# Kernel optimization log

Measured on AMD Instinct MI355X. Metric: run time of the kernel, lower is better.

The kernel has to match this reference:

```python
import jax, jax.numpy as jnp
import numpy as np

OUTDIM, INPUTDIM, DEGREE = 64, 512, 8


def setup_inputs() -> dict:
    key = jax.random.key(0)
    k1, k2 = jax.random.split(key)
    x = jax.random.normal(k1, (16, 4096, INPUTDIM), dtype=jnp.float32)
    # torch.randn(outdim, inputdim, degree) / (sqrt(inputdim)*sqrt(degree))
    coeffs = jax.random.normal(k2, (OUTDIM, INPUTDIM, DEGREE), dtype=jnp.float32)
    coeffs = coeffs / (np.sqrt(INPUTDIM) * np.sqrt(DEGREE))
    bias = jnp.zeros((1, OUTDIM), dtype=jnp.float32)
    return {"x": x, "coeffs": coeffs, "bias": bias}


def _legendre_basis(xn, degree):
    # Iterative (memoized) Legendre recurrence; xn in [-1, 1], shape [N, I].
    Ps = [jnp.ones_like(xn)]
    if degree > 1:
        Ps.append(xn)
    for n in range(2, degree):
        Ps.append(((2.0 * n - 1.0) * xn * Ps[-1] - (n - 1.0) * Ps[-2]) / n)
    return jnp.stack(Ps, axis=-1)  # [N, I, D]


def reference(x, coeffs, bias):
    outdim, inputdim, degree = coeffs.shape
    outshape = x.shape[:-1] + (outdim,)
    x2 = x.reshape(-1, inputdim)                      # [N, I]
    xmin, xmax = x2.min(), x2.max()                   # global min-max normalize
    xn = 2.0 * (x2 - xmin) / (xmax - xmin) - 1.0
    P = _legendre_basis(xn, degree)                   # [N, I, D]
    y = jnp.einsum("nid,oid->no", P, coeffs)          # contract input & degree
    y = y + bias                                      # [N, O]
    return y.reshape(outshape)
```

## Files before the change

kernel.cpp:

```cpp
#include <hip/hip_runtime.h>
#include <math.h>


typedef __bf16 bf16x8 __attribute__((ext_vector_type(8)));
typedef float f32x4 __attribute__((ext_vector_type(4)));

__global__ __launch_bounds__(256) void k_minmax_partial(
    const float4* __restrict__ x4, int n4, float* __restrict__ pmn, float* __restrict__ pmx)
{
  float mn = 3.4e38f, mx = -3.4e38f;
  int stride = gridDim.x * 256;
  for (int i = blockIdx.x * 256 + threadIdx.x; i < n4; i += stride) {
    float4 v = x4[i];
    mn = fminf(mn, fminf(fminf(v.x, v.y), fminf(v.z, v.w)));
    mx = fmaxf(mx, fmaxf(fmaxf(v.x, v.y), fmaxf(v.z, v.w)));
  }
  #pragma unroll
  for (int off = 32; off > 0; off >>= 1) {
    mn = fminf(mn, __shfl_down(mn, off));
    mx = fmaxf(mx, __shfl_down(mx, off));
  }
  __shared__ float smn[4], smx[4];
  int w = threadIdx.x >> 6;
  if ((threadIdx.x & 63) == 0) { smn[w] = mn; smx[w] = mx; }
  __syncthreads();
  if (threadIdx.x == 0) {
    pmn[blockIdx.x] = fminf(fminf(smn[0], smn[1]), fminf(smn[2], smn[3]));
    pmx[blockIdx.x] = fmaxf(fmaxf(smx[0], smx[1]), fmaxf(smx[2], smx[3]));
  }
}

__global__ __launch_bounds__(256) void k_minmax_final(
    const float* __restrict__ pmn, const float* __restrict__ pmx, int nb, float* __restrict__ so)
{
  float mn = 3.4e38f, mx = -3.4e38f;
  for (int i = threadIdx.x; i < nb; i += 256) {
    mn = fminf(mn, pmn[i]);
    mx = fmaxf(mx, pmx[i]);
  }
  #pragma unroll
  for (int off = 32; off > 0; off >>= 1) {
    mn = fminf(mn, __shfl_down(mn, off));
    mx = fmaxf(mx, __shfl_down(mx, off));
  }
  __shared__ float smn[4], smx[4];
  int w = threadIdx.x >> 6;
  if ((threadIdx.x & 63) == 0) { smn[w] = mn; smx[w] = mx; }
  __syncthreads();
  if (threadIdx.x == 0) {
    mn = fminf(fminf(smn[0], smn[1]), fminf(smn[2], smn[3]));
    mx = fmaxf(fmaxf(smx[0], smx[1]), fmaxf(smx[2], smx[3]));
    float r = mx - mn;
    so[0] = 2.0f / r;
    so[1] = -2.0f * mn / r - 1.0f;
  }
}

__global__ __launch_bounds__(256) void k_prepB(const float* __restrict__ coeffs,
                                               bf16x8* __restrict__ Bws)
{
  int t = blockIdx.x * 256 + threadIdx.x;
  int lane = t & 63;
  int tile = t >> 6;
  int ct = tile & 3;
  int kt = tile >> 2;
  int i = kt * 4 + (lane >> 4);
  int o = ct * 16 + (lane & 15);
  const float4* cp = (const float4*)(coeffs + ((size_t)o * 512 + i) * 8);
  float4 c0 = cp[0], c1 = cp[1];
  bf16x8 v;
  v[0] = (__bf16)c0.x; v[1] = (__bf16)c0.y; v[2] = (__bf16)c0.z; v[3] = (__bf16)c0.w;
  v[4] = (__bf16)c1.x; v[5] = (__bf16)c1.y; v[6] = (__bf16)c1.z; v[7] = (__bf16)c1.w;
  Bws[t] = v;
}

#define LSTRIDE 36
__global__ __launch_bounds__(128, 1) void k_main(
    const float* __restrict__ x, const bf16x8* __restrict__ Bws,
    const float* __restrict__ bias, const float* __restrict__ so,
    float* __restrict__ y)
{
  __shared__ float xs[2][128 * LSTRIDE];

  const float s = so[0], off = so[1];
  const int t    = threadIdx.x;
  const int lane = t & 63;
  const int w    = t >> 6;
  const int m    = lane & 15;
  const int quad = lane >> 4;
  const size_t blockRow = (size_t)blockIdx.x * 128;

  const int srow = t >> 3;
  const int scol = (t & 7) * 4;
  const float* xg = x + blockRow * 512;

  int rbase[4];
  #pragma unroll
  for (int f = 0; f < 4; ++f) rbase[f] = (w * 64 + f * 16 + m) * LSTRIDE + quad;

  const bf16x8* Bp = Bws + lane;

  f32x4 acc[4][4];
  #pragma unroll
  for (int f = 0; f < 4; ++f)
    #pragma unroll
    for (int ct = 0; ct < 4; ++ct) acc[f][ct] = (f32x4){0.f, 0.f, 0.f, 0.f};

  const float c3a = 5.f / 3.f,  c3b = 2.f / 3.f;
  const float c6a = 11.f / 6.f, c6b = 5.f / 6.f;
  const float c7a = 13.f / 7.f, c7b = 6.f / 7.f;

  {
    #pragma unroll
    for (int p = 0; p < 8; ++p) {
      float4 v = *(const float4*)(xg + (size_t)(srow + 16 * p) * 512 + scol);
      *(float4*)&xs[0][(srow + 16 * p) * LSTRIDE + scol] = v;
    }
  }
  __syncthreads();

  bf16x8 Bq[4][4];
  #pragma unroll
  for (int ct = 0; ct < 4; ++ct) {
    Bq[0][ct] = Bp[(size_t)(0 * 4 + ct) * 64];
    Bq[1][ct] = Bp[(size_t)(1 * 4 + ct) * 64];
  }

  for (int c = 0; c < 16; ++c) {
    const float* xr = xs[c & 1];
    float*       xw = xs[(c & 1) ^ 1];

    float4 st[8];
    if (c < 15) {
      const float* gp = xg + (c + 1) * 32;
      #pragma unroll
      for (int p = 0; p < 8; ++p)
        st[p] = *(const float4*)(gp + (size_t)(srow + 16 * p) * 512 + scol);
    }

    float xv[2][4];
    #pragma unroll
    for (int f = 0; f < 4; ++f) xv[0][f] = xr[rbase[f]];

    #pragma unroll
    for (int ktl = 0; ktl < 8; ++ktl) {
      const int kt = c * 8 + ktl;

      {
        const int kp = (kt + 2) & 127;
        const bf16x8* bpk = Bp + (size_t)kp * 256;
        #pragma unroll
        for (int ct = 0; ct < 4; ++ct) Bq[(ktl + 2) & 3][ct] = bpk[ct * 64];
      }
      if (ktl < 7) {
        #pragma unroll
        for (int f = 0; f < 4; ++f)
          xv[(ktl + 1) & 1][f] = xr[rbase[f] + (ktl + 1) * 4];
      }

      bf16x8 a[4];
      #pragma unroll
      for (int f = 0; f < 4; ++f) {
        float xn = fmaf(xv[ktl & 1][f], s, off);
        float p2 = fmaf(1.5f * xn, xn, -0.5f);
        float p3 = fmaf(c3a * xn, p2, -(c3b * xn));
        float p4 = fmaf(1.75f * xn, p3, -(0.75f * p2));
        float p5 = fmaf(1.8f * xn, p4, -(0.8f * p3));
        float p6 = fmaf(c6a * xn, p5, -(c6b * p4));
        float p7 = fmaf(c7a * xn, p6, -(c7b * p5));
        bf16x8 av;
        av[0] = (__bf16)1.0f; av[1] = (__bf16)xn; av[2] = (__bf16)p2; av[3] = (__bf16)p3;
        av[4] = (__bf16)p4;   av[5] = (__bf16)p5; av[6] = (__bf16)p6; av[7] = (__bf16)p7;
        a[f] = av;
      }

      #pragma unroll
      for (int f = 0; f < 4; ++f)
        #pragma unroll
        for (int ct = 0; ct < 4; ++ct)
          acc[f][ct] = __builtin_amdgcn_mfma_f32_16x16x32_bf16(a[f], Bq[ktl & 3][ct], acc[f][ct], 0, 0, 0);
    }

    if (c < 15) {
      #pragma unroll
      for (int p = 0; p < 8; ++p)
        *(float4*)&xw[(srow + 16 * p) * LSTRIDE + scol] = st[p];
    }
    __syncthreads();
  }

  float bv0 = bias[m], bv1 = bias[16 + m], bv2 = bias[32 + m], bv3 = bias[48 + m];
  #pragma unroll
  for (int f = 0; f < 4; ++f) {
    float* yp = y + (blockRow + w * 64 + f * 16 + quad * 4) * 64 + m;
    #pragma unroll
    for (int r = 0; r < 4; ++r) {
      float* ypr = yp + r * 64;
      ypr[0]  = acc[f][0][r] + bv0;
      ypr[16] = acc[f][1][r] + bv1;
      ypr[32] = acc[f][2][r] + bv2;
      ypr[48] = acc[f][3][r] + bv3;
    }
  }
}

__global__ __launch_bounds__(256) void k_main_simple(
    const float* __restrict__ x, const float* __restrict__ coeffs,
    const float* __restrict__ bias, const float* __restrict__ so, float* __restrict__ y)
{
  const float s = so[0], off = so[1];
  const int lane = threadIdx.x & 63;
  const int w    = threadIdx.x >> 6;
  const int m    = lane & 15;
  const int quad = lane >> 4;
  const int rowA = blockIdx.x * 64 + w * 16 + m;
  const float* xp = x + (size_t)rowA * 512 + quad;

  f32x4 acc0 = {0.f,0.f,0.f,0.f}, acc1 = acc0, acc2 = acc0, acc3 = acc0;
  const float c3a = 5.f/3.f, c3b = 2.f/3.f, c6a = 11.f/6.f, c6b = 5.f/6.f, c7a = 13.f/7.f, c7b = 6.f/7.f;

  for (int kt = 0; kt < 128; ++kt) {
    float xv = xp[kt * 4];
    int i = kt * 4 + quad;
    bf16x8 b[4];
    #pragma unroll
    for (int ct = 0; ct < 4; ++ct) {
      const float* cp = coeffs + ((size_t)(ct * 16 + m) * 512 + i) * 8;
      #pragma unroll
      for (int j = 0; j < 8; ++j) b[ct][j] = (__bf16)cp[j];
    }
    float xn = fmaf(xv, s, off);
    float p2 = fmaf(1.5f * xn, xn, -0.5f);
    float p3 = fmaf(c3a * xn, p2, -(c3b * xn));
    float p4 = fmaf(1.75f * xn, p3, -(0.75f * p2));
    float p5 = fmaf(1.8f * xn, p4, -(0.8f * p3));
    float p6 = fmaf(c6a * xn, p5, -(c6b * p4));
    float p7 = fmaf(c7a * xn, p6, -(c7b * p5));
    bf16x8 a;
    a[0] = (__bf16)1.0f; a[1] = (__bf16)xn; a[2] = (__bf16)p2; a[3] = (__bf16)p3;
    a[4] = (__bf16)p4;   a[5] = (__bf16)p5; a[6] = (__bf16)p6; a[7] = (__bf16)p7;
    acc0 = __builtin_amdgcn_mfma_f32_16x16x32_bf16(a, b[0], acc0, 0, 0, 0);
    acc1 = __builtin_amdgcn_mfma_f32_16x16x32_bf16(a, b[1], acc1, 0, 0, 0);
    acc2 = __builtin_amdgcn_mfma_f32_16x16x32_bf16(a, b[2], acc2, 0, 0, 0);
    acc3 = __builtin_amdgcn_mfma_f32_16x16x32_bf16(a, b[3], acc3, 0, 0, 0);
  }
  float b0v = bias[m], b1v = bias[16+m], b2v = bias[32+m], b3v = bias[48+m];
  float* yp = y + ((size_t)(blockIdx.x * 64 + w * 16 + quad * 4)) * 64 + m;
  #pragma unroll
  for (int r = 0; r < 4; ++r) {
    yp[r*64+ 0] = acc0[r] + b0v;
    yp[r*64+16] = acc1[r] + b1v;
    yp[r*64+32] = acc2[r] + b2v;
    yp[r*64+48] = acc3[r] + b3v;
  }
}

extern "C" void kernel_launch(void* const* d_in, const int* in_sizes, int n_in,
                              void* d_out, int out_size, void* d_ws, size_t ws_size,
                              hipStream_t stream)
{
  const float* x      = (const float*)d_in[0];
  const float* coeffs = (const float*)d_in[1];
  const float* bias   = (const float*)d_in[2];
  float* y = (float*)d_out;

  long nx = (long)in_sizes[0];
  int  N  = (int)(nx / 512);
  int  n4 = (int)(nx / 4);

  float*  so  = (float*)d_ws;
  float*  pmn = (float*)d_ws + 16;
  float*  pmx = pmn + 4096;
  bf16x8* Bws = (bf16x8*)((char*)d_ws + 65536);

  const int MMB = 2048;
  k_minmax_partial<<<MMB, 256, 0, stream>>>((const float4*)x, n4, pmn, pmx);
  k_minmax_final<<<1, 256, 0, stream>>>(pmn, pmx, MMB, so);

  bool pre = ws_size >= (size_t)(65536 + 4096 * 64 * 2 + 4096);
  if (pre) {
    k_prepB<<<128, 256, 0, stream>>>(coeffs, Bws);
    k_main<<<N / 128, 128, 0, stream>>>(x, Bws, bias, so, y);
  } else {
    k_main_simple<<<N / 64, 256, 0, stream>>>(x, coeffs, bias, so, y);
  }
}
```

Before: 287.5 us.

## Split K across waves with LDS reduction, merge prep kernels, rescale Legendre recurrence

The main kernel now uses 64-row blocks of 4 waves. Each wave handles a quarter of the input dimension over the same rows, stages its x slice in a private LDS buffer with no per-chunk barriers, and the partial accumulators are summed through shared memory at the end. The min-max finalize and coefficient conversion are merged into one launch. The Legendre recurrence is rewritten in monic (scaled) form, with the scale factors folded into the bf16 coefficients, which cuts the FLOPs per element. This aims to raise occupancy and parallelism, remove block-wide syncs and one launch, at the cost of an LDS reduction and a different bf16 rounding profile. The simple fallback path now reads unconverted coeffs while the prep kernel runs unconditionally, so the fallback still works.

```diff
diff --git a/kernel.cpp b/kernel.cpp
--- a/kernel.cpp
+++ b/kernel.cpp
@@ -30,57 +30,63 @@
   }
 }
 
-__global__ __launch_bounds__(256) void k_minmax_final(
-    const float* __restrict__ pmn, const float* __restrict__ pmx, int nb, float* __restrict__ so)
-{
-  float mn = 3.4e38f, mx = -3.4e38f;
-  for (int i = threadIdx.x; i < nb; i += 256) {
-    mn = fminf(mn, pmn[i]);
-    mx = fmaxf(mx, pmx[i]);
-  }
-  #pragma unroll
-  for (int off = 32; off > 0; off >>= 1) {
-    mn = fminf(mn, __shfl_down(mn, off));
-    mx = fmaxf(mx, __shfl_down(mx, off));
-  }
-  __shared__ float smn[4], smx[4];
-  int w = threadIdx.x >> 6;
-  if ((threadIdx.x & 63) == 0) { smn[w] = mn; smx[w] = mx; }
-  __syncthreads();
-  if (threadIdx.x == 0) {
-    mn = fminf(fminf(smn[0], smn[1]), fminf(smn[2], smn[3]));
-    mx = fmaxf(fmaxf(smx[0], smx[1]), fmaxf(smx[2], smx[3]));
-    float r = mx - mn;
-    so[0] = 2.0f / r;
-    so[1] = -2.0f * mn / r - 1.0f;
-  }
-}
-
-__global__ __launch_bounds__(256) void k_prepB(const float* __restrict__ coeffs,
-                                               bf16x8* __restrict__ Bws)
-{
-  int t = blockIdx.x * 256 + threadIdx.x;
-  int lane = t & 63;
-  int tile = t >> 6;
-  int ct = tile & 3;
-  int kt = tile >> 2;
-  int i = kt * 4 + (lane >> 4);
-  int o = ct * 16 + (lane & 15);
-  const float4* cp = (const float4*)(coeffs + ((size_t)o * 512 + i) * 8);
-  float4 c0 = cp[0], c1 = cp[1];
-  bf16x8 v;
-  v[0] = (__bf16)c0.x; v[1] = (__bf16)c0.y; v[2] = (__bf16)c0.z; v[3] = (__bf16)c0.w;
-  v[4] = (__bf16)c1.x; v[5] = (__bf16)c1.y; v[6] = (__bf16)c1.z; v[7] = (__bf16)c1.w;
-  Bws[t] = v;
-}
-
-#define LSTRIDE 36
-__global__ __launch_bounds__(128, 1) void k_main(
+__global__ __launch_bounds__(256) void k_prep_final(
+    const float* __restrict__ coeffs, bf16x8* __restrict__ Bws,
+    const float* __restrict__ pmn, const float* __restrict__ pmx, int nb,
+    float* __restrict__ so)
+{
+  if (blockIdx.x < 128) {
+    int t = blockIdx.x * 256 + threadIdx.x;
+    int lane = t & 63;
+    int tile = t >> 6;
+    int ct = tile & 3;
+    int kt = tile >> 2;
+    int i = kt * 4 + (lane >> 4);
+    int o = ct * 16 + (lane & 15);
+    const float4* cp = (const float4*)(coeffs + ((size_t)o * 512 + i) * 8);
+    float4 c0 = cp[0], c1 = cp[1];
+    bf16x8 v;
+    v[0] = (__bf16)(c0.x);
+    v[1] = (__bf16)(c0.y);
+    v[2] = (__bf16)(c0.z * 1.5f);
+    v[3] = (__bf16)(c0.w * 2.5f);
+    v[4] = (__bf16)(c1.x * 4.375f);
+    v[5] = (__bf16)(c1.y * 7.875f);
+    v[6] = (__bf16)(c1.z * 14.4375f);
+    v[7] = (__bf16)(c1.w * 26.8125f);
+    Bws[(size_t)(kt * 4 + ct) * 64 + lane] = v;
+  } else {
+    float mn = 3.4e38f, mx = -3.4e38f;
+    for (int i = threadIdx.x; i < nb; i += 256) {
+      mn = fminf(mn, pmn[i]);
+      mx = fmaxf(mx, pmx[i]);
+    }
+    #pragma unroll
+    for (int off = 32; off > 0; off >>= 1) {
+      mn = fminf(mn, __shfl_down(mn, off));
+      mx = fmaxf(mx, __shfl_down(mx, off));
+    }
+    __shared__ float smn[4], smx[4];
+    int w = threadIdx.x >> 6;
+    if ((threadIdx.x & 63) == 0) { smn[w] = mn; smx[w] = mx; }
+    __syncthreads();
+    if (threadIdx.x == 0) {
+      mn = fminf(fminf(smn[0], smn[1]), fminf(smn[2], smn[3]));
+      mx = fmaxf(fmaxf(smx[0], smx[1]), fmaxf(smx[2], smx[3]));
+      float r = mx - mn;
+      so[0] = 2.0f / r;
+      so[1] = -2.0f * mn / r - 1.0f;
+    }
+  }
+}
+
+#define LSTW 20
+__global__ __launch_bounds__(256, 3) void k_main(
     const float* __restrict__ x, const bf16x8* __restrict__ Bws,
     const float* __restrict__ bias, const float* __restrict__ so,
     float* __restrict__ y)
 {
-  __shared__ float xs[2][128 * LSTRIDE];
+  __shared__ char smem[49152];
 
   const float s = so[0], off = so[1];
   const int t    = threadIdx.x;
@@ -88,17 +94,16 @@
   const int w    = t >> 6;
   const int m    = lane & 15;
   const int quad = lane >> 4;
-  const size_t blockRow = (size_t)blockIdx.x * 128;
-
-  const int srow = t >> 3;
-  const int scol = (t & 7) * 4;
-  const float* xg = x + blockRow * 512;
-
-  int rbase[4];
-  #pragma unroll
-  for (int f = 0; f < 4; ++f) rbase[f] = (w * 64 + f * 16 + m) * LSTRIDE + quad;
-
-  const bf16x8* Bp = Bws + lane;
+  const size_t blockRow = (size_t)blockIdx.x * 64;
+
+  float* xsw = (float*)(smem + w * (2 * 64 * LSTW * 4));
+  const float* xg = x + (blockRow + lane) * 512 + w * 128;
+
+  int rb[4];
+  #pragma unroll
+  for (int f = 0; f < 4; ++f) rb[f] = (f * 16 + m) * LSTW + quad;
+
+  const bf16x8* Bp = Bws + (size_t)w * 32 * 256 + lane;
 
   f32x4 acc[4][4];
   #pragma unroll
@@ -106,71 +111,64 @@
     #pragma unroll
     for (int ct = 0; ct < 4; ++ct) acc[f][ct] = (f32x4){0.f, 0.f, 0.f, 0.f};
 
-  const float c3a = 5.f / 3.f,  c3b = 2.f / 3.f;
-  const float c6a = 11.f / 6.f, c6b = 5.f / 6.f;
-  const float c7a = 13.f / 7.f, c7b = 6.f / 7.f;
-
-  {
-    #pragma unroll
-    for (int p = 0; p < 8; ++p) {
-      float4 v = *(const float4*)(xg + (size_t)(srow + 16 * p) * 512 + scol);
-      *(float4*)&xs[0][(srow + 16 * p) * LSTRIDE + scol] = v;
-    }
-  }
-  __syncthreads();
+  const float C2 = 0.33333334f, C3 = 0.26666668f, C4 = 0.25714287f;
+  const float C5 = 0.25396827f, C6 = 0.25252524f, C7 = 0.25174826f;
+
+  float4 st[4];
+  #pragma unroll
+  for (int p = 0; p < 4; ++p) st[p] = *(const float4*)(xg + p * 4);
+  #pragma unroll
+  for (int p = 0; p < 4; ++p) *(float4*)&xsw[lane * LSTW + p * 4] = st[p];
 
   bf16x8 Bq[4][4];
   #pragma unroll
   for (int ct = 0; ct < 4; ++ct) {
-    Bq[0][ct] = Bp[(size_t)(0 * 4 + ct) * 64];
-    Bq[1][ct] = Bp[(size_t)(1 * 4 + ct) * 64];
-  }
-
-  for (int c = 0; c < 16; ++c) {
-    const float* xr = xs[c & 1];
-    float*       xw = xs[(c & 1) ^ 1];
-
-    float4 st[8];
-    if (c < 15) {
-      const float* gp = xg + (c + 1) * 32;
-      #pragma unroll
-      for (int p = 0; p < 8; ++p)
-        st[p] = *(const float4*)(gp + (size_t)(srow + 16 * p) * 512 + scol);
+    Bq[0][ct] = Bp[ct * 64];
+    Bq[1][ct] = Bp[256 + ct * 64];
+  }
+
+  for (int c = 0; c < 8; ++c) {
+    float* xr = xsw + (c & 1) * (64 * LSTW);
+
+    if (c < 7) {
+      const float* gp = xg + (c + 1) * 16;
+      #pragma unroll
+      for (int p = 0; p < 4; ++p) st[p] = *(const float4*)(gp + p * 4);
     }
 
     float xv[2][4];
     #pragma unroll
-    for (int f = 0; f < 4; ++f) xv[0][f] = xr[rbase[f]];
-
-    #pragma unroll
-    for (int ktl = 0; ktl < 8; ++ktl) {
-      const int kt = c * 8 + ktl;
+    for (int f = 0; f < 4; ++f) xv[0][f] = xr[rb[f]];
+
+    #pragma unroll
+    for (int ktl = 0; ktl < 4; ++ktl) {
+      const int l = c * 4 + ktl;
 
       {
-        const int kp = (kt + 2) & 127;
+        const int kp = (l + 2) & 31;
         const bf16x8* bpk = Bp + (size_t)kp * 256;
         #pragma unroll
         for (int ct = 0; ct < 4; ++ct) Bq[(ktl + 2) & 3][ct] = bpk[ct * 64];
       }
-      if (ktl < 7) {
+      if (ktl < 3) {
         #pragma unroll
         for (int f = 0; f < 4; ++f)
-          xv[(ktl + 1) & 1][f] = xr[rbase[f] + (ktl + 1) * 4];
+          xv[(ktl + 1) & 1][f] = xr[rb[f] + (ktl + 1) * 4];
       }
 
       bf16x8 a[4];
       #pragma unroll
       for (int f = 0; f < 4; ++f) {
         float xn = fmaf(xv[ktl & 1][f], s, off);
-        float p2 = fmaf(1.5f * xn, xn, -0.5f);
-        float p3 = fmaf(c3a * xn, p2, -(c3b * xn));
-        float p4 = fmaf(1.75f * xn, p3, -(0.75f * p2));
-        float p5 = fmaf(1.8f * xn, p4, -(0.8f * p3));
-        float p6 = fmaf(c6a * xn, p5, -(c6b * p4));
-        float p7 = fmaf(c7a * xn, p6, -(c7b * p5));
+        float s2 = fmaf(xn, xn, -C2);
+        float s3 = (s2 - C3) * xn;
+        float s4 = fmaf(xn, s3, -(C4 * s2));
+        float s5 = fmaf(xn, s4, -(C5 * s3));
+        float s6 = fmaf(xn, s5, -(C6 * s4));
+        float s7 = fmaf(xn, s6, -(C7 * s5));
         bf16x8 av;
-        av[0] = (__bf16)1.0f; av[1] = (__bf16)xn; av[2] = (__bf16)p2; av[3] = (__bf16)p3;
-        av[4] = (__bf16)p4;   av[5] = (__bf16)p5; av[6] = (__bf16)p6; av[7] = (__bf16)p7;
+        av[0] = (__bf16)1.0f; av[1] = (__bf16)xn; av[2] = (__bf16)s2; av[3] = (__bf16)s3;
+        av[4] = (__bf16)s4;   av[5] = (__bf16)s5; av[6] = (__bf16)s6; av[7] = (__bf16)s7;
         a[f] = av;
       }
 
@@ -181,25 +179,46 @@
           acc[f][ct] = __builtin_amdgcn_mfma_f32_16x16x32_bf16(a[f], Bq[ktl & 3][ct], acc[f][ct], 0, 0, 0);
     }
 
-    if (c < 15) {
-      #pragma unroll
-      for (int p = 0; p < 8; ++p)
-        *(float4*)&xw[(srow + 16 * p) * LSTRIDE + scol] = st[p];
-    }
-    __syncthreads();
-  }
-
-  float bv0 = bias[m], bv1 = bias[16 + m], bv2 = bias[32 + m], bv3 = bias[48 + m];
-  #pragma unroll
-  for (int f = 0; f < 4; ++f) {
-    float* yp = y + (blockRow + w * 64 + f * 16 + quad * 4) * 64 + m;
-    #pragma unroll
-    for (int r = 0; r < 4; ++r) {
-      float* ypr = yp + r * 64;
-      ypr[0]  = acc[f][0][r] + bv0;
-      ypr[16] = acc[f][1][r] + bv1;
-      ypr[32] = acc[f][2][r] + bv2;
-      ypr[48] = acc[f][3][r] + bv3;
+    if (c < 7) {
+      float* xw = xsw + ((c + 1) & 1) * (64 * LSTW);
+      #pragma unroll
+      for (int p = 0; p < 4; ++p) *(float4*)&xw[lane * LSTW + p * 4] = st[p];
+    }
+  }
+
+  __syncthreads();
+  f32x4* red = (f32x4*)smem;
+  if (w > 0) {
+    #pragma unroll
+    for (int f = 0; f < 4; ++f)
+      #pragma unroll
+      for (int ct = 0; ct < 4; ++ct)
+        red[(size_t)(w - 1) * 1024 + (f * 4 + ct) * 64 + lane] = acc[f][ct];
+  }
+  __syncthreads();
+  if (w == 0) {
+    #pragma unroll
+    for (int f = 0; f < 4; ++f)
+      #pragma unroll
+      for (int ct = 0; ct < 4; ++ct) {
+        f32x4 v = acc[f][ct];
+        v += red[(f * 4 + ct) * 64 + lane];
+        v += red[1024 + (f * 4 + ct) * 64 + lane];
+        v += red[2048 + (f * 4 + ct) * 64 + lane];
+        acc[f][ct] = v;
+      }
+    float bv0 = bias[m], bv1 = bias[16 + m], bv2 = bias[32 + m], bv3 = bias[48 + m];
+    #pragma unroll
+    for (int f = 0; f < 4; ++f) {
+      float* yp = y + (blockRow + f * 16 + quad * 4) * 64 + m;
+      #pragma unroll
+      for (int r = 0; r < 4; ++r) {
+        float* ypr = yp + r * 64;
+        ypr[0]  = acc[f][0][r] + bv0;
+        ypr[16] = acc[f][1][r] + bv1;
+        ypr[32] = acc[f][2][r] + bv2;
+        ypr[48] = acc[f][3][r] + bv3;
+      }
     }
   }
 }
@@ -275,12 +294,11 @@
 
   const int MMB = 2048;
   k_minmax_partial<<<MMB, 256, 0, stream>>>((const float4*)x, n4, pmn, pmx);
-  k_minmax_final<<<1, 256, 0, stream>>>(pmn, pmx, MMB, so);
 
   bool pre = ws_size >= (size_t)(65536 + 4096 * 64 * 2 + 4096);
+  k_prep_final<<<129, 256, 0, stream>>>(coeffs, Bws, pmn, pmx, MMB, so);
   if (pre) {
-    k_prepB<<<128, 256, 0, stream>>>(coeffs, Bws);
-    k_main<<<N / 128, 128, 0, stream>>>(x, Bws, bias, so, y);
+    k_main<<<N / 64, 256, 0, stream>>>(x, Bws, bias, so, y);
   } else {
     k_main_simple<<<N / 64, 256, 0, stream>>>(x, coeffs, bias, so, y);
   }
```

Measured after the change: 252.3 us. 12.3% less time.
